# Performance work log

Hardware: AMD Instinct MI355X
Metric: run time of the kernel (lower is better)

## Reference

```python
import jax, jax.numpy as jnp
import numpy as np

# Mamba2 dims (match init_kwargs)
DM = 1024          # d_model
EXPAND = 2
D_INNER = EXPAND * DM            # 2048 (== d_ssm)
HEADDIM = 64
NHEADS = D_INNER // HEADDIM      # 32
DSTATE = 128
NGROUPS = 1
DCONV = 4
CONV_DIM = D_INNER + 2 * NGROUPS * DSTATE        # 2304
D_IN_PROJ = 2 * D_INNER + 2 * NGROUPS * DSTATE + NHEADS  # 4384
BATCH, SEQ = 4, 1024
EPS = 1e-5


def setup_inputs() -> dict:
    key = jax.random.key(0)
    ks = jax.random.split(key, 8)
    x = jax.random.normal(ks[0], (BATCH, SEQ, DM), dtype=jnp.float32)
    in_proj_w = jax.random.normal(ks[1], (D_IN_PROJ, DM), dtype=jnp.float32) * 0.02
    conv_w = jax.random.normal(ks[2], (CONV_DIM, 1, DCONV), dtype=jnp.float32) * 0.2
    conv_b = jnp.zeros((CONV_DIM,), dtype=jnp.float32)
    # dt_bias = inv_softplus(dt) with dt ~ logU[dt_min, dt_max]
    dt = jnp.exp(jax.random.uniform(ks[3], (NHEADS,)) * (np.log(0.1) - np.log(0.001)) + np.log(0.001))
    dt_bias = dt + jnp.log(-jnp.expm1(-dt))
    # A ~ U[1, 16], A_log = log(A)
    A_log = jnp.log(jax.random.uniform(ks[4], (NHEADS,), minval=1.0, maxval=16.0))
    D = jnp.ones((NHEADS,), dtype=jnp.float32)
    norm_w = jnp.ones((D_INNER,), dtype=jnp.float32)
    out_proj_w = jax.random.normal(ks[5], (DM, D_INNER), dtype=jnp.float32) * 0.02
    return {"x": x, "in_proj_w": in_proj_w, "conv_w": conv_w, "conv_b": conv_b,
            "dt_bias": dt_bias, "A_log": A_log, "D": D, "norm_w": norm_w,
            "out_proj_w": out_proj_w}


def _mamba2_forward(x, in_proj_w, conv_w, conv_b, dt_bias, A_log, D, norm_w, out_proj_w):
    B, L, _ = x.shape
    zxbcdt = jnp.einsum('bld,ed->ble', x, in_proj_w)  # (B,L,D_IN_PROJ)
    z = zxbcdt[..., :D_INNER]
    xBC = zxbcdt[..., D_INNER:D_INNER + CONV_DIM]
    dt_raw = zxbcdt[..., D_INNER + CONV_DIM:]         # (B,L,NHEADS)

    # causal depthwise conv1d + silu
    xt = jnp.transpose(xBC, (0, 2, 1))                # (B, CONV_DIM, L)
    conv = jax.lax.conv_general_dilated(
        xt, conv_w, window_strides=(1,), padding=[(DCONV - 1, 0)],
        dimension_numbers=('NCH', 'OIH', 'NCH'), feature_group_count=CONV_DIM)
    conv = conv + conv_b[None, :, None]
    xBC = jnp.transpose(jax.nn.silu(conv), (0, 2, 1))  # (B,L,CONV_DIM)

    x_ssm = xBC[..., :D_INNER].reshape(B, L, NHEADS, HEADDIM)
    Bm = xBC[..., D_INNER:D_INNER + NGROUPS * DSTATE].reshape(B, L, NGROUPS, DSTATE)
    Cm = xBC[..., D_INNER + NGROUPS * DSTATE:].reshape(B, L, NGROUPS, DSTATE)

    dt = jax.nn.softplus(dt_raw + dt_bias)            # (B,L,H)
    A = -jnp.exp(A_log)                               # (H,)
    dA = jnp.exp(dt * A)                              # (B,L,H)
    dtx = dt[..., None] * x_ssm                       # (B,L,H,P)

    rep = NHEADS // NGROUPS
    Bh = jnp.repeat(Bm, rep, axis=2)                  # (B,L,H,N)
    Ch = jnp.repeat(Cm, rep, axis=2)

    def step(h, inp):
        dA_t, dtx_t, B_t, C_t = inp
        h = dA_t[:, :, None, None] * h + dtx_t[..., None] * B_t[:, :, None, :]
        y = jnp.einsum('bhpn,bhn->bhp', h, C_t)
        return h, y

    h0 = jnp.zeros((B, NHEADS, HEADDIM, DSTATE), dtype=x.dtype)
    xs = (jnp.transpose(dA, (1, 0, 2)),
          jnp.transpose(dtx, (1, 0, 2, 3)),
          jnp.transpose(Bh, (1, 0, 2, 3)),
          jnp.transpose(Ch, (1, 0, 2, 3)))
    _, ys = jax.lax.scan(step, h0, xs)                # (L,B,H,P)
    y = jnp.transpose(ys, (1, 0, 2, 3)) + D[None, None, :, None] * x_ssm
    y = y.reshape(B, L, D_INNER)

    # gated RMSNorm (norm_before_gate=False): normalize(y * silu(z)) * w
    yz = y * jax.nn.silu(z)
    yz = yz * jax.lax.rsqrt(jnp.mean(yz * yz, axis=-1, keepdims=True) + EPS) * norm_w

    return jnp.einsum('bld,ed->ble', yz, out_proj_w)  # (B,L,DM)


def reference(x, in_proj_w, conv_w, conv_b, dt_bias, A_log, D, norm_w, out_proj_w):
    return _mamba2_forward(x, in_proj_w, conv_w, conv_b, dt_bias, A_log, D, norm_w, out_proj_w)
```

## Files before the change

kernel.cpp:

```cpp
#include <hip/hip_runtime.h>
#include <hip/hip_bf16.h>

#define DM        1024
#define D_INNER   2048
#define NHEADS    32
#define HEADDIM   64
#define DSTATE    128
#define DCONV     4
#define CONV_DIM  (D_INNER + 2*DSTATE)
#define D_IN_PROJ (2*D_INNER + 2*DSTATE + NHEADS)
#define NPAD_IN   4480
#define BATCH     4
#define SEQ       1024
#define NROWS     (BATCH*SEQ)
#define EPSF      1e-5f
#define CHUNK     128
#define NCHUNK    (SEQ/CHUNK)
#define BH        (BATCH*NHEADS)

#define OFF_ZX   ((size_t)0)
#define OFF_XBC  ((size_t)(NROWS)*D_IN_PROJ)
#define OFF_DT   (OFF_XBC + (size_t)NROWS*CONV_DIM)
#define OFF_DA   (OFF_DT  + (size_t)NROWS*NHEADS)
#define OFF_Y    (OFF_DA  + (size_t)NROWS*NHEADS)
#define FLOAT_END (OFF_Y + (size_t)NROWS*D_INNER)
#define SOFF_XB   ((size_t)0)
#define SOFF_W1B  (SOFF_XB  + (size_t)NROWS*DM)
#define SOFF_W2B  (SOFF_W1B + (size_t)NPAD_IN*DM)
#define SOFF_YZB  (SOFF_W2B + (size_t)DM*D_INNER)
#define HD_SHORTS ((size_t)NCHUNK*BH*HEADDIM*DSTATE)

typedef float  vf4   __attribute__((ext_vector_type(4)));
typedef short  s16x8 __attribute__((ext_vector_type(8)));
typedef short  s16x4 __attribute__((ext_vector_type(4)));
typedef __bf16 bf16x8 __attribute__((ext_vector_type(8)));

__device__ __forceinline__ float sigmoidf_(float x) { return 1.f / (1.f + expf(-x)); }

__device__ __forceinline__ short f2bf(float f) {
    unsigned u = __builtin_bit_cast(unsigned, f);
    u += 0x7fffu + ((u >> 16) & 1u);
    return (short)(u >> 16);
}
__device__ __forceinline__ float bf2f(short s) {
    unsigned u = ((unsigned)(unsigned short)s) << 16;
    return __builtin_bit_cast(float, u);
}
__device__ __forceinline__ bf16x8 as_bf(s16x8 v) { return __builtin_bit_cast(bf16x8, v); }
#define MFMA(a,b,c) __builtin_amdgcn_mfma_f32_16x16x32_bf16(as_bf(a), as_bf(b), (c), 0, 0, 0)

__device__ __forceinline__ void gload16(const short* g, short* l) {
    __builtin_amdgcn_global_load_lds(
        (const __attribute__((address_space(1))) unsigned int*)g,
        (__attribute__((address_space(3))) unsigned int*)l, 16, 0, 0);
}

__device__ __forceinline__ int swz_idx(int r, int kc) {
    return r * 128 + (((kc) ^ (r & 7)) << 3);
}
__device__ __forceinline__ int swz64_idx(int r, int c) {
    return r * 64 + (((c) ^ (r & 7)) << 3);
}
__device__ __forceinline__ void stage_tile(const float* __restrict__ g, int gstride,
                                           short* __restrict__ lds, int rows,
                                           int tid, int nthr) {
    for (int s = tid; s < rows * 16; s += nthr) {
        int r = s >> 4, c = s & 15;
        const float* p = g + (size_t)r * gstride + c * 8;
        float4 v0 = *(const float4*)p, v1 = *(const float4*)(p + 4);
        s16x8 o;
        o[0]=f2bf(v0.x); o[1]=f2bf(v0.y); o[2]=f2bf(v0.z); o[3]=f2bf(v0.w);
        o[4]=f2bf(v1.x); o[5]=f2bf(v1.y); o[6]=f2bf(v1.z); o[7]=f2bf(v1.w);
        *(s16x8*)&lds[swz_idx(r, c)] = o;
    }
}

__global__ __launch_bounds__(256) void cvt_bf16(const float* __restrict__ src,
                                                short* __restrict__ dst,
                                                int n_src, int n_dst) {
    int i = (blockIdx.x * 256 + threadIdx.x) * 4;
    if (i >= n_dst) return;
    s16x4 o;
    if (i + 3 < n_src) {
        float4 v = *(const float4*)(src + i);
        o[0] = f2bf(v.x); o[1] = f2bf(v.y); o[2] = f2bf(v.z); o[3] = f2bf(v.w);
    } else {
        #pragma unroll
        for (int j = 0; j < 4; ++j) o[j] = (i + j < n_src) ? f2bf(src[i + j]) : (short)0;
    }
    *(s16x4*)(dst + i) = o;
}

__global__ __launch_bounds__(256) void gemm_mfma(const short* __restrict__ A,
                                                 const short* __restrict__ B,
                                                 float* __restrict__ C,
                                                 int M, int K, int Nout) {
    __shared__ short smem[16384];
    const int tid = threadIdx.x;
    const int bm = blockIdx.y * 128, bn = blockIdx.x * 128;
    const int lane = tid & 63, lr = lane & 15, lg = lane >> 4;
    const int w = tid >> 6, wm = w >> 1, wn = w & 1;

    const short* ga[4]; const short* gb[4];
    short* la[4]; short* lb[4];
    #pragma unroll
    for (int t = 0; t < 4; ++t) {
        int s = t * 256 + tid;
        int r = s >> 3;
        int c = (s & 7) ^ (r & 7);
        ga[t] = A + (size_t)(bm + r) * K + c * 8;
        gb[t] = B + (size_t)(bn + r) * K + c * 8;
        la[t] = &smem[s * 8];
        lb[t] = &smem[8192 + s * 8];
    }

    vf4 acc[4][4] = {};

    for (int k0 = 0; k0 < K; k0 += 64) {
        __syncthreads();
        #pragma unroll
        for (int t = 0; t < 4; ++t) gload16(ga[t] + k0, la[t]);
        #pragma unroll
        for (int t = 0; t < 4; ++t) gload16(gb[t] + k0, lb[t]);
        __syncthreads();
        #pragma unroll
        for (int kk = 0; kk < 2; ++kk) {
            const int co = ((kk * 4 + lg) ^ (lr & 7)) * 8;
            s16x8 av[4], bv[4];
            #pragma unroll
            for (int f = 0; f < 4; ++f) {
                av[f] = *(const s16x8*)&smem[(wm * 64 + f * 16 + lr) * 64 + co];
                bv[f] = *(const s16x8*)&smem[8192 + (wn * 64 + f * 16 + lr) * 64 + co];
            }
            #pragma unroll
            for (int i = 0; i < 4; ++i)
                #pragma unroll
                for (int j = 0; j < 4; ++j)
                    acc[i][j] = MFMA(av[i], bv[j], acc[i][j]);
        }
    }

    #pragma unroll
    for (int i = 0; i < 4; ++i) {
        int row = bm + wm * 64 + i * 16 + lg * 4;
        #pragma unroll
        for (int j = 0; j < 4; ++j) {
            int col = bn + wn * 64 + j * 16 + lr;
            if (col < Nout) {
                float* cp = C + (size_t)row * Nout + col;
                #pragma unroll
                for (int q = 0; q < 4; ++q) cp[(size_t)q * Nout] = acc[i][j][q];
            }
        }
    }
}

__global__ __launch_bounds__(256) void conv_silu(const float* __restrict__ zx,
                                                 const float* __restrict__ cw,
                                                 const float* __restrict__ cb,
                                                 float* __restrict__ xBC) {
    int idx = blockIdx.x * 256 + threadIdx.x;
    if (idx >= NROWS * CONV_DIM) return;
    int c  = idx % CONV_DIM;
    int bl = idx / CONV_DIM;
    int b  = bl / SEQ;
    int l  = bl % SEQ;

    float w0 = cw[c*4+0], w1 = cw[c*4+1], w2 = cw[c*4+2], w3 = cw[c*4+3];
    const float* base = zx + (size_t)b * SEQ * D_IN_PROJ + D_INNER + c;

    float acc = cb[c];
    if (l >= 3) acc = fmaf(base[(size_t)(l-3) * D_IN_PROJ], w0, acc);
    if (l >= 2) acc = fmaf(base[(size_t)(l-2) * D_IN_PROJ], w1, acc);
    if (l >= 1) acc = fmaf(base[(size_t)(l-1) * D_IN_PROJ], w2, acc);
    acc = fmaf(base[(size_t)l * D_IN_PROJ], w3, acc);

    xBC[idx] = acc * sigmoidf_(acc);
}

__global__ __launch_bounds__(256) void dt_da(const float* __restrict__ zx,
                                             const float* __restrict__ dt_bias,
                                             float* __restrict__ dt) {
    int idx = blockIdx.x * 256 + threadIdx.x;
    if (idx >= NROWS * NHEADS) return;
    int h  = idx & (NHEADS - 1);
    int bl = idx >> 5;
    float u = zx[(size_t)bl * D_IN_PROJ + D_INNER + CONV_DIM + h] + dt_bias[h];
    float d = (u > 20.f) ? u : log1pf(expf(u));
    dt[idx] = d;
}

#define L_CT 0
#define L_XT 0
#define L_BT 16384
#define L_BW 32768
#define L_XN 49152
__global__ __launch_bounds__(1024) void ssm_mfma_a(const float* __restrict__ xBC,
                                                   const float* __restrict__ dt,
                                                   const float* __restrict__ A_log,
                                                   const float* __restrict__ Dp,
                                                   float* __restrict__ y,
                                                   short* __restrict__ hd16,
                                                   float* __restrict__ datot) {
    __shared__ short sm[57344];
    __shared__ float dtl[128], lcs[128];
    int blk = blockIdx.x;
    int h = blk & 31, k = (blk >> 5) & (NCHUNK - 1), b = blk >> 8;
    int tid = threadIdx.x, w = tid >> 6, lane = tid & 63, lr = lane & 15, lg = lane >> 4;
    int bl0 = b * SEQ + k * CHUNK;
    const float* xrow = xBC + (size_t)bl0 * CONV_DIM;

    if (tid < 128) dtl[tid] = dt[(size_t)(bl0 + tid) * NHEADS + h];

    stage_tile(xrow + D_INNER + DSTATE, CONV_DIM, sm + L_CT, 128, tid, 1024);
    stage_tile(xrow + D_INNER,          CONV_DIM, sm + L_BT, 128, tid, 1024);
    {
        int r = tid >> 3, c = tid & 7;
        const float* p = xrow + (size_t)r * CONV_DIM + h * HEADDIM + c * 8;
        float4 v0 = *(const float4*)p, v1 = *(const float4*)(p + 4);
        s16x8 o;
        o[0]=f2bf(v0.x); o[1]=f2bf(v0.y); o[2]=f2bf(v0.z); o[3]=f2bf(v0.w);
        o[4]=f2bf(v1.x); o[5]=f2bf(v1.y); o[6]=f2bf(v1.z); o[7]=f2bf(v1.w);
        *(s16x8*)&sm[L_XN + swz64_idx(r, c)] = o;
    }
    __syncthreads();

    float Ah = -__expf(A_log[h]);
    if (w == 0) {
        float a = dtl[lane], bb = dtl[64 + lane];
        #pragma unroll
        for (int d = 1; d < 64; d <<= 1) { float v = __shfl_up(a, d);  if (lane >= d) a  += v; }
        #pragma unroll
        for (int d = 1; d < 64; d <<= 1) { float v = __shfl_up(bb, d); if (lane >= d) bb += v; }
        bb += __shfl(a, 63);
        lcs[lane]      = Ah * a;
        lcs[64 + lane] = Ah * bb;
        if (lane == 63) datot[k * BH + b * NHEADS + h] = __expf(Ah * bb);
    }

    vf4 g[4] = {};
    const int rb = (w & 7) * 16, cb = (w >> 3) * 64;
    #pragma unroll
    for (int ks = 0; ks < 4; ++ks) {
        int kc = ks * 4 + lg;
        s16x8 av = *(const s16x8*)&sm[L_CT + swz_idx(rb + lr, kc)];
        #pragma unroll
        for (int jf = 0; jf < 4; ++jf) {
            s16x8 bv = *(const s16x8*)&sm[L_BT + swz_idx(cb + jf * 16 + lr, kc)];
            g[jf] = MFMA(av, bv, g[jf]);
        }
    }
    __syncthreads();

    float lcLast = lcs[127];

    {
        int p = tid & 63, c2 = tid >> 6;
        s16x8 o;
        #pragma unroll
        for (int jj = 0; jj < 8; ++jj) {
            int j = c2 * 8 + jj;
            float xv = bf2f(sm[L_XN + swz64_idx(j, p >> 3) + (p & 7)]);
            o[jj] = f2bf(dtl[j] * xv);
        }
        *(s16x8*)&sm[L_XT + swz_idx(p, c2)] = o;
    }
    for (int s = tid; s < 2048; s += 1024) {
        int n = s & 127, c = s >> 7;
        s16x8 o;
        #pragma unroll
        for (int jj = 0; jj < 8; ++jj) {
            int j = c * 8 + jj;
            float bv = bf2f(sm[L_BT + swz_idx(j, n >> 3) + (n & 7)]);
            o[jj] = f2bf(bv * __expf(lcLast - lcs[j]));
        }
        *(s16x8*)&sm[L_BW + swz_idx(n, c)] = o;
    }
    __syncthreads();

    #pragma unroll
    for (int jf = 0; jf < 4; ++jf)
        #pragma unroll
        for (int q = 0; q < 4; ++q) {
            int t = rb + lg * 4 + q;
            int j = cb + jf * 16 + lr;
            float v = (j <= t) ? g[jf][q] * __expf(lcs[t] - lcs[j]) : 0.f;
            sm[L_BT + swz_idx(t, j >> 3) + (j & 7)] = f2bf(v);
        }
    __syncthreads();

    vf4 yi[2] = {};
    vf4 hdl[2] = {};
    const int rb2 = (w & 7) * 16, prb = (w >> 3) * 32;
    const int hrb = (w & 3) * 16, hcb = (w >> 2) * 32;
    #pragma unroll
    for (int ks = 0; ks < 4; ++ks) {
        int kc = ks * 4 + lg;
        s16x8 am = *(const s16x8*)&sm[L_BT + swz_idx(rb2 + lr, kc)];
        s16x8 ax = *(const s16x8*)&sm[L_XT + swz_idx(hrb + lr, kc)];
        #pragma unroll
        for (int jf = 0; jf < 2; ++jf) {
            s16x8 bx = *(const s16x8*)&sm[L_XT + swz_idx(prb + jf * 16 + lr, kc)];
            s16x8 bw = *(const s16x8*)&sm[L_BW + swz_idx(hcb + jf * 16 + lr, kc)];
            yi[jf]  = MFMA(am, bx, yi[jf]);
            hdl[jf] = MFMA(ax, bw, hdl[jf]);
        }
    }

    float Dh = Dp[h];
    #pragma unroll
    for (int jf = 0; jf < 2; ++jf)
        #pragma unroll
        for (int q = 0; q < 4; ++q) {
            int t = rb2 + lg * 4 + q;
            int p = prb + jf * 16 + lr;
            float xv = xrow[(size_t)t * CONV_DIM + h * HEADDIM + p];
            y[(size_t)(bl0 + t) * D_INNER + h * HEADDIM + p] = yi[jf][q] + Dh * xv;
        }
    size_t hb = ((size_t)k * BH + b * NHEADS + h) * (HEADDIM * DSTATE);
    #pragma unroll
    for (int jf = 0; jf < 2; ++jf)
        #pragma unroll
        for (int q = 0; q < 4; ++q) {
            int p = hrb + lg * 4 + q;
            int n = hcb + jf * 16 + lr;
            hd16[hb + p * DSTATE + n] = f2bf(hdl[jf][q]);
        }
}

__global__ __launch_bounds__(512) void ssm_state_b(short* __restrict__ hd16,
                                                   const float* __restrict__ datot) {
    int bh = blockIdx.x;
    int base = threadIdx.x * 16;
    float hs[16];
    #pragma unroll
    for (int i = 0; i < 16; ++i) hs[i] = 0.f;
    #pragma unroll
    for (int k = 0; k < NCHUNK; ++k) {
        size_t off = ((size_t)k * BH + bh) * (HEADDIM * DSTATE) + base;
        float da = datot[k * BH + bh];
        s16x8 d0 = *(const s16x8*)&hd16[off], d1 = *(const s16x8*)&hd16[off + 8];
        s16x8 o0, o1;
        #pragma unroll
        for (int i = 0; i < 8; ++i) { o0[i] = f2bf(hs[i]); o1[i] = f2bf(hs[8 + i]); }
        *(s16x8*)&hd16[off] = o0; *(s16x8*)&hd16[off + 8] = o1;
        #pragma unroll
        for (int i = 0; i < 8; ++i) {
            hs[i]     = fmaf(da, hs[i],     bf2f(d0[i]));
            hs[8 + i] = fmaf(da, hs[8 + i], bf2f(d1[i]));
        }
    }
}

__global__ __launch_bounds__(512) void ssm_mfma_c(const float* __restrict__ xBC,
                                                  const float* __restrict__ dt,
                                                  const float* __restrict__ A_log,
                                                  const short* __restrict__ hd16,
                                                  float* __restrict__ y) {
    int blk = blockIdx.x;
    int h = blk & 31, k = (blk >> 5) & (NCHUNK - 1), b = blk >> 8;
    if (k == 0) return;
    __shared__ short sm[16384];
    __shared__ float dtl[128], lcs[128];
    int tid = threadIdx.x, w = tid >> 6, lane = tid & 63, lr = lane & 15, lg = lane >> 4;
    int bl0 = b * SEQ + k * CHUNK;
    const float* xrow = xBC + (size_t)bl0 * CONV_DIM;

    if (tid < 128) dtl[tid] = dt[(size_t)(bl0 + tid) * NHEADS + h];
    __syncthreads();
    stage_tile(xrow + D_INNER + DSTATE, CONV_DIM, sm, 128, tid, 512);
    float Ah = -__expf(A_log[h]);
    __syncthreads();
    if (w == 0) {
        float a = dtl[lane], bb = dtl[64 + lane];
        #pragma unroll
        for (int d = 1; d < 64; d <<= 1) { float v = __shfl_up(a, d);  if (lane >= d) a  += v; }
        #pragma unroll
        for (int d = 1; d < 64; d <<= 1) { float v = __shfl_up(bb, d); if (lane >= d) bb += v; }
        bb += __shfl(a, 63);
        lcs[lane]      = Ah * a;
        lcs[64 + lane] = Ah * bb;
    }
    __syncthreads();

    const short* hin = hd16 + ((size_t)k * BH + b * NHEADS + h) * (HEADDIM * DSTATE);
    vf4 yi[2][2] = {};
    const int rb = (w & 3) * 32, prb = (w >> 2) * 32;
    #pragma unroll
    for (int ks = 0; ks < 4; ++ks) {
        int kc = ks * 4 + lg;
        s16x8 av[2], bv[2];
        #pragma unroll
        for (int i = 0; i < 2; ++i)  { int r = rb + i * 16 + lr; av[i] = *(const s16x8*)&sm[swz_idx(r, kc)]; }
        #pragma unroll
        for (int jf = 0; jf < 2; ++jf){
            int p = prb + jf * 16 + lr;
            bv[jf] = *(const s16x8*)&hin[p * DSTATE + ks * 32 + lg * 8];
        }
        #pragma unroll
        for (int i = 0; i < 2; ++i)
            #pragma unroll
            for (int jf = 0; jf < 2; ++jf)
                yi[i][jf] = MFMA(av[i], bv[jf], yi[i][jf]);
    }
    #pragma unroll
    for (int i = 0; i < 2; ++i)
        #pragma unroll
        for (int jf = 0; jf < 2; ++jf)
            #pragma unroll
            for (int q = 0; q < 4; ++q) {
                int t = rb + i * 16 + lg * 4 + q;
                int p = prb + jf * 16 + lr;
                float* yp = y + (size_t)(bl0 + t) * D_INNER + h * HEADDIM + p;
                *yp = fmaf(__expf(lcs[t]), yi[i][jf][q], *yp);
            }
}

__global__ __launch_bounds__(256) void gate_rmsnorm(const float* __restrict__ y,
                                                    const float* __restrict__ zx,
                                                    const float* __restrict__ nw,
                                                    short* __restrict__ yzb) {
    int bl = blockIdx.x;
    const float* yr = y + (size_t)bl * D_INNER;
    const float* zr = zx + (size_t)bl * D_IN_PROJ;
    int e0 = threadIdx.x * 8;

    float4 y0 = *(const float4*)(yr + e0);
    float4 y1 = *(const float4*)(yr + e0 + 4);
    float4 z0 = *(const float4*)(zr + e0);
    float4 z1 = *(const float4*)(zr + e0 + 4);

    float v[8];
    float zz[8] = {z0.x, z0.y, z0.z, z0.w, z1.x, z1.y, z1.z, z1.w};
    float yy[8] = {y0.x, y0.y, y0.z, y0.w, y1.x, y1.y, y1.z, y1.w};
    float ss = 0.f;
    #pragma unroll
    for (int i = 0; i < 8; ++i) {
        v[i] = yy[i] * zz[i] * sigmoidf_(zz[i]);
        ss = fmaf(v[i], v[i], ss);
    }
    ss += __shfl_xor(ss, 1);  ss += __shfl_xor(ss, 2);  ss += __shfl_xor(ss, 4);
    ss += __shfl_xor(ss, 8);  ss += __shfl_xor(ss, 16); ss += __shfl_xor(ss, 32);
    __shared__ float red[4];
    int wave = threadIdx.x >> 6;
    if ((threadIdx.x & 63) == 0) red[wave] = ss;
    __syncthreads();
    ss = red[0] + red[1] + red[2] + red[3];

    float scale = rsqrtf(ss * (1.f / D_INNER) + EPSF);
    s16x8 o;
    #pragma unroll
    for (int i = 0; i < 8; ++i) o[i] = f2bf(v[i] * scale * nw[e0 + i]);
    *(s16x8*)(yzb + (size_t)bl * D_INNER + e0) = o;
}

extern "C" void kernel_launch(void* const* d_in, const int* in_sizes, int n_in,
                              void* d_out, int out_size, void* d_ws, size_t ws_size,
                              hipStream_t stream) {
    const float* x        = (const float*)d_in[0];
    const float* in_w     = (const float*)d_in[1];
    const float* conv_w   = (const float*)d_in[2];
    const float* conv_b   = (const float*)d_in[3];
    const float* dt_bias  = (const float*)d_in[4];
    const float* A_log    = (const float*)d_in[5];
    const float* Dp       = (const float*)d_in[6];
    const float* norm_w   = (const float*)d_in[7];
    const float* out_w    = (const float*)d_in[8];
    float* out            = (float*)d_out;

    float* ws   = (float*)d_ws;
    float* zx   = ws + OFF_ZX;
    float* xBC  = ws + OFF_XBC;
    float* dt   = ws + OFF_DT;
    float* y    = ws + OFF_Y;
    short* sb   = (short*)(ws + FLOAT_END);
    short* xb   = sb + SOFF_XB;
    short* w1b  = sb + SOFF_W1B;
    short* w2b  = sb + SOFF_W2B;
    short* yzb  = sb + SOFF_YZB;
    short* hd16  = xb;
    float* datot = (float*)(hd16 + HD_SHORTS);

    {
        int n = NROWS * DM;
        cvt_bf16<<<n / 4 / 256, 256, 0, stream>>>(x, xb, n, n);
        int ns = D_IN_PROJ * DM, nd = NPAD_IN * DM;
        cvt_bf16<<<nd / 4 / 256, 256, 0, stream>>>(in_w, w1b, ns, nd);
        int n2 = DM * D_INNER;
        cvt_bf16<<<n2 / 4 / 256, 256, 0, stream>>>(out_w, w2b, n2, n2);
    }
    {
        dim3 grid(NPAD_IN / 128, NROWS / 128);
        gemm_mfma<<<grid, 256, 0, stream>>>(xb, w1b, zx, NROWS, DM, D_IN_PROJ);
    }
    {
        int total = NROWS * CONV_DIM;
        conv_silu<<<(total + 255) / 256, 256, 0, stream>>>(zx, conv_w, conv_b, xBC);
    }
    {
        int total = NROWS * NHEADS;
        dt_da<<<(total + 255) / 256, 256, 0, stream>>>(zx, dt_bias, dt);
    }
    ssm_mfma_a<<<BATCH * NCHUNK * NHEADS, 1024, 0, stream>>>(xBC, dt, A_log, Dp, y, hd16, datot);
    ssm_state_b<<<BH, 512, 0, stream>>>(hd16, datot);
    ssm_mfma_c<<<BATCH * NCHUNK * NHEADS, 512, 0, stream>>>(xBC, dt, A_log, hd16, y);
    gate_rmsnorm<<<NROWS, 256, 0, stream>>>(y, zx, norm_w, yzb);
    {
        dim3 grid(DM / 128, NROWS / 128);
        gemm_mfma<<<grid, 256, 0, stream>>>(yzb, w2b, out, NROWS, D_INNER, DM);
    }
}
```

Baseline: 337.7 us.

## Store in-projection output as bf16 and remap blocks across XCDs

The in-projection GEMM now writes its output as bf16 instead of fp32, which halves the traffic for writing zx and for the later reads by conv, dt and gate kernels. Those consumers convert bf16 back to float on load. The GEMM and SSM kernels also remap the 1D block index so that consecutive tiles land on the same XCD (groups of 8), aiming for better L2 reuse. The bf16 intermediate adds rounding error to z, xBC and dt before the scan.

Measured after the change: 309.1 us. -8.5%, faster.

```diff
diff --git a/kernel.cpp b/kernel.cpp
--- a/kernel.cpp
+++ b/kernel.cpp
@@ -49,6 +49,10 @@
 __device__ __forceinline__ bf16x8 as_bf(s16x8 v) { return __builtin_bit_cast(bf16x8, v); }
 #define MFMA(a,b,c) __builtin_amdgcn_mfma_f32_16x16x32_bf16(as_bf(a), as_bf(b), (c), 0, 0, 0)
 
+template <typename T> __device__ __forceinline__ T cvt_out(float v);
+template <> __device__ __forceinline__ float cvt_out<float>(float v) { return v; }
+template <> __device__ __forceinline__ short cvt_out<short>(float v) { return f2bf(v); }
+
 __device__ __forceinline__ void gload16(const short* g, short* l) {
     __builtin_amdgcn_global_load_lds(
         (const __attribute__((address_space(1))) unsigned int*)g,
@@ -91,13 +95,16 @@
     *(s16x4*)(dst + i) = o;
 }
 
+template <typename OutT>
 __global__ __launch_bounds__(256) void gemm_mfma(const short* __restrict__ A,
                                                  const short* __restrict__ B,
-                                                 float* __restrict__ C,
-                                                 int M, int K, int Nout) {
+                                                 OutT* __restrict__ C,
+                                                 int K, int Nout, int nbx) {
     __shared__ short smem[16384];
     const int tid = threadIdx.x;
-    const int bm = blockIdx.y * 128, bn = blockIdx.x * 128;
+    const int cpx = gridDim.x >> 3;
+    const int wgid = (blockIdx.x & 7) * cpx + (blockIdx.x >> 3);
+    const int bm = (wgid / nbx) * 128, bn = (wgid % nbx) * 128;
     const int lane = tid & 63, lr = lane & 15, lg = lane >> 4;
     const int w = tid >> 6, wm = w >> 1, wn = w & 1;
 
@@ -147,15 +154,15 @@
         for (int j = 0; j < 4; ++j) {
             int col = bn + wn * 64 + j * 16 + lr;
             if (col < Nout) {
-                float* cp = C + (size_t)row * Nout + col;
+                OutT* cp = C + (size_t)row * Nout + col;
                 #pragma unroll
-                for (int q = 0; q < 4; ++q) cp[(size_t)q * Nout] = acc[i][j][q];
+                for (int q = 0; q < 4; ++q) cp[(size_t)q * Nout] = cvt_out<OutT>(acc[i][j][q]);
             }
         }
     }
 }
 
-__global__ __launch_bounds__(256) void conv_silu(const float* __restrict__ zx,
+__global__ __launch_bounds__(256) void conv_silu(const short* __restrict__ zx,
                                                  const float* __restrict__ cw,
                                                  const float* __restrict__ cb,
                                                  float* __restrict__ xBC) {
@@ -167,25 +174,25 @@
     int l  = bl % SEQ;
 
     float w0 = cw[c*4+0], w1 = cw[c*4+1], w2 = cw[c*4+2], w3 = cw[c*4+3];
-    const float* base = zx + (size_t)b * SEQ * D_IN_PROJ + D_INNER + c;
+    const short* base = zx + (size_t)b * SEQ * D_IN_PROJ + D_INNER + c;
 
     float acc = cb[c];
-    if (l >= 3) acc = fmaf(base[(size_t)(l-3) * D_IN_PROJ], w0, acc);
-    if (l >= 2) acc = fmaf(base[(size_t)(l-2) * D_IN_PROJ], w1, acc);
-    if (l >= 1) acc = fmaf(base[(size_t)(l-1) * D_IN_PROJ], w2, acc);
-    acc = fmaf(base[(size_t)l * D_IN_PROJ], w3, acc);
+    if (l >= 3) acc = fmaf(bf2f(base[(size_t)(l-3) * D_IN_PROJ]), w0, acc);
+    if (l >= 2) acc = fmaf(bf2f(base[(size_t)(l-2) * D_IN_PROJ]), w1, acc);
+    if (l >= 1) acc = fmaf(bf2f(base[(size_t)(l-1) * D_IN_PROJ]), w2, acc);
+    acc = fmaf(bf2f(base[(size_t)l * D_IN_PROJ]), w3, acc);
 
     xBC[idx] = acc * sigmoidf_(acc);
 }
 
-__global__ __launch_bounds__(256) void dt_da(const float* __restrict__ zx,
+__global__ __launch_bounds__(256) void dt_da(const short* __restrict__ zx,
                                              const float* __restrict__ dt_bias,
                                              float* __restrict__ dt) {
     int idx = blockIdx.x * 256 + threadIdx.x;
     if (idx >= NROWS * NHEADS) return;
     int h  = idx & (NHEADS - 1);
     int bl = idx >> 5;
-    float u = zx[(size_t)bl * D_IN_PROJ + D_INNER + CONV_DIM + h] + dt_bias[h];
+    float u = bf2f(zx[(size_t)bl * D_IN_PROJ + D_INNER + CONV_DIM + h]) + dt_bias[h];
     float d = (u > 20.f) ? u : log1pf(expf(u));
     dt[idx] = d;
 }
@@ -204,7 +211,7 @@
                                                    float* __restrict__ datot) {
     __shared__ short sm[57344];
     __shared__ float dtl[128], lcs[128];
-    int blk = blockIdx.x;
+    int blk = (blockIdx.x & 7) * (gridDim.x >> 3) + (blockIdx.x >> 3);
     int h = blk & 31, k = (blk >> 5) & (NCHUNK - 1), b = blk >> 8;
     int tid = threadIdx.x, w = tid >> 6, lane = tid & 63, lr = lane & 15, lg = lane >> 4;
     int bl0 = b * SEQ + k * CHUNK;
@@ -357,7 +364,7 @@
                                                   const float* __restrict__ A_log,
                                                   const short* __restrict__ hd16,
                                                   float* __restrict__ y) {
-    int blk = blockIdx.x;
+    int blk = (blockIdx.x & 7) * (gridDim.x >> 3) + (blockIdx.x >> 3);
     int h = blk & 31, k = (blk >> 5) & (NCHUNK - 1), b = blk >> 8;
     if (k == 0) return;
     __shared__ short sm[16384];
@@ -417,26 +424,25 @@
 }
 
 __global__ __launch_bounds__(256) void gate_rmsnorm(const float* __restrict__ y,
-                                                    const float* __restrict__ zx,
+                                                    const short* __restrict__ zxs,
                                                     const float* __restrict__ nw,
                                                     short* __restrict__ yzb) {
     int bl = blockIdx.x;
     const float* yr = y + (size_t)bl * D_INNER;
-    const float* zr = zx + (size_t)bl * D_IN_PROJ;
+    const short* zr = zxs + (size_t)bl * D_IN_PROJ;
     int e0 = threadIdx.x * 8;
 
     float4 y0 = *(const float4*)(yr + e0);
     float4 y1 = *(const float4*)(yr + e0 + 4);
-    float4 z0 = *(const float4*)(zr + e0);
-    float4 z1 = *(const float4*)(zr + e0 + 4);
+    s16x8 zv = *(const s16x8*)(zr + e0);
 
     float v[8];
-    float zz[8] = {z0.x, z0.y, z0.z, z0.w, z1.x, z1.y, z1.z, z1.w};
     float yy[8] = {y0.x, y0.y, y0.z, y0.w, y1.x, y1.y, y1.z, y1.w};
     float ss = 0.f;
     #pragma unroll
     for (int i = 0; i < 8; ++i) {
-        v[i] = yy[i] * zz[i] * sigmoidf_(zz[i]);
+        float zz = bf2f(zv[i]);
+        v[i] = yy[i] * zz * sigmoidf_(zz);
         ss = fmaf(v[i], v[i], ss);
     }
     ss += __shfl_xor(ss, 1);  ss += __shfl_xor(ss, 2);  ss += __shfl_xor(ss, 4);
@@ -469,7 +475,7 @@
     float* out            = (float*)d_out;
 
     float* ws   = (float*)d_ws;
-    float* zx   = ws + OFF_ZX;
+    short* zxs  = (short*)(ws + OFF_ZX);
     float* xBC  = ws + OFF_XBC;
     float* dt   = ws + OFF_DT;
     float* y    = ws + OFF_Y;
@@ -489,24 +495,20 @@
         int n2 = DM * D_INNER;
         cvt_bf16<<<n2 / 4 / 256, 256, 0, stream>>>(out_w, w2b, n2, n2);
     }
-    {
-        dim3 grid(NPAD_IN / 128, NROWS / 128);
-        gemm_mfma<<<grid, 256, 0, stream>>>(xb, w1b, zx, NROWS, DM, D_IN_PROJ);
-    }
+    gemm_mfma<short><<<(NPAD_IN / 128) * (NROWS / 128), 256, 0, stream>>>(
+        xb, w1b, zxs, DM, D_IN_PROJ, NPAD_IN / 128);
     {
         int total = NROWS * CONV_DIM;
-        conv_silu<<<(total + 255) / 256, 256, 0, stream>>>(zx, conv_w, conv_b, xBC);
+        conv_silu<<<(total + 255) / 256, 256, 0, stream>>>(zxs, conv_w, conv_b, xBC);
     }
     {
         int total = NROWS * NHEADS;
-        dt_da<<<(total + 255) / 256, 256, 0, stream>>>(zx, dt_bias, dt);
+        dt_da<<<(total + 255) / 256, 256, 0, stream>>>(zxs, dt_bias, dt);
     }
     ssm_mfma_a<<<BATCH * NCHUNK * NHEADS, 1024, 0, stream>>>(xBC, dt, A_log, Dp, y, hd16, datot);
     ssm_state_b<<<BH, 512, 0, stream>>>(hd16, datot);
     ssm_mfma_c<<<BATCH * NCHUNK * NHEADS, 512, 0, stream>>>(xBC, dt, A_log, hd16, y);
-    gate_rmsnorm<<<NROWS, 256, 0, stream>>>(y, zx, norm_w, yzb);
-    {
-        dim3 grid(DM / 128, NROWS / 128);
-        gemm_mfma<<<grid, 256, 0, stream>>>(yzb, w2b, out, NROWS, D_INNER, DM);
-    }
-}
+    gate_rmsnorm<<<NROWS, 256, 0, stream>>>(y, zxs, norm_w, yzb);
+    gemm_mfma<float><<<(DM / 128) * (NROWS / 128), 256, 0, stream>>>(
+        yzb, w2b, out, D_INNER, DM, DM / 128);
+}
```
